# Kernel optimization log

Hardware: AMD Instinct MI355X
Metric: run time of the kernel (lower is better)

## Reference

```python
import jax, jax.numpy as jnp
import numpy as np

HIDDEN = 2048
NUM_HEADS = 8
NUM_KV_HEADS = 2
HEAD_DIM = 256
ROPE_BASE = 1e6
EPS = 1e-6
B, S = 2, 2048


def rms_norm(x, w, eps=EPS):
    # normalize over last dim (head_dim), per-head
    var = jnp.mean(jnp.square(x), axis=-1, keepdims=True)
    return x * jax.lax.rsqrt(var + eps) * w


def rope(x, positions, base=ROPE_BASE):
    # neox-style rotate-half RoPE over full head_dim. x: [B,S,H,D], positions: [B,S]
    d = x.shape[-1]
    inv_freq = 1.0 / (base ** (jnp.arange(0, d, 2, dtype=jnp.float32) / d))
    freqs = positions.astype(jnp.float32)[..., None] * inv_freq  # [B,S,D/2]
    cos = jnp.cos(freqs)[:, :, None, :]
    sin = jnp.sin(freqs)[:, :, None, :]
    x1, x2 = x[..., : d // 2], x[..., d // 2 :]
    return jnp.concatenate([x1 * cos - x2 * sin, x2 * cos + x1 * sin], axis=-1)


def setup_inputs() -> dict:
    key = jax.random.key(0)
    k1, k2, k3 = jax.random.split(key, 3)
    hidden_states = jax.random.normal(k1, (B, S, HIDDEN), dtype=jnp.float32)
    positions = jnp.broadcast_to(jnp.arange(S, dtype=jnp.int32), (B, S))
    qkv_out = (NUM_HEADS + 2 * NUM_KV_HEADS) * HEAD_DIM
    w_qkv = jax.random.normal(k2, (HIDDEN, qkv_out), dtype=jnp.float32) * (HIDDEN ** -0.5)
    w_o = jax.random.normal(k3, (NUM_HEADS * HEAD_DIM, HIDDEN), dtype=jnp.float32) * ((NUM_HEADS * HEAD_DIM) ** -0.5)
    q_norm_w = jnp.ones((HEAD_DIM,), dtype=jnp.float32)
    k_norm_w = jnp.ones((HEAD_DIM,), dtype=jnp.float32)
    return {"hidden_states": hidden_states, "positions": positions, "w_qkv": w_qkv,
            "w_o": w_o, "q_norm_w": q_norm_w, "k_norm_w": k_norm_w}


def reference(hidden_states, positions, w_qkv, w_o, q_norm_w, k_norm_w):
    b, s, _ = hidden_states.shape
    q_size = NUM_HEADS * HEAD_DIM
    kv_size = NUM_KV_HEADS * HEAD_DIM
    qkv = hidden_states @ w_qkv  # [B,S,q+2kv]
    q, k, v = jnp.split(qkv, [q_size, q_size + kv_size], axis=-1)
    q = q.reshape(b, s, NUM_HEADS, HEAD_DIM)
    k = k.reshape(b, s, NUM_KV_HEADS, HEAD_DIM)
    v = v.reshape(b, s, NUM_KV_HEADS, HEAD_DIM)
    # per-head RMSNorm; v_norm has no learned scale (weight fixed to ones)
    q = rms_norm(q, q_norm_w)
    k = rms_norm(k, k_norm_w)
    v = rms_norm(v, jnp.ones((HEAD_DIM,), dtype=v.dtype))
    # RoPE
    q = rope(q, positions)
    k = rope(k, positions)
    # GQA: repeat kv heads
    g = NUM_HEADS // NUM_KV_HEADS
    k = jnp.repeat(k, g, axis=2)
    v = jnp.repeat(v, g, axis=2)
    # causal attention with scaling = 1.0 (as in module)
    scores = jnp.einsum("bqhd,bkhd->bhqk", q, k)
    mask = jnp.tril(jnp.ones((s, s), dtype=bool))
    scores = jnp.where(mask, scores, jnp.finfo(scores.dtype).min)
    probs = jax.nn.softmax(scores, axis=-1)
    attn = jnp.einsum("bhqk,bkhd->bqhd", probs, v).reshape(b, s, NUM_HEADS * HEAD_DIM)
    return attn @ w_o
```

## Files before the change

kernel.cpp:

```cpp
#include <hip/hip_runtime.h>


#define HID  2048
#define NH   8
#define NKV  2
#define HD   256
#define SB   2048
#define BB   2
#define MTOK (BB * SB)
#define NQKV ((NH + 2 * NKV) * HD)

typedef _Float16  f16x8 __attribute__((ext_vector_type(8)));
typedef float     f32x4 __attribute__((ext_vector_type(4)));

__device__ __forceinline__ unsigned short f2h(float f) {
  _Float16 h = (_Float16)f;
  return __builtin_bit_cast(unsigned short, h);
}

__device__ __forceinline__ void async_copy16(const unsigned short* g, unsigned short* l) {
  __builtin_amdgcn_global_load_lds(
      (const __attribute__((address_space(1))) unsigned int*)g,
      (__attribute__((address_space(3))) unsigned int*)l, 16, 0, 0);
}

__device__ __forceinline__ int swz4(int r) { return (r + (r >> 2)) & 3; }

template <int OUT_MODE>
__global__ __launch_bounds__(256) void gemm_bt(const unsigned short* __restrict__ A,
                                               const unsigned short* __restrict__ Bt,
                                               void* __restrict__ Cg,
                                               int M, int N, int K) {
  __shared__ unsigned short Ash[128 * 32];
  __shared__ unsigned short Bsh[128 * 32];
  const int t = threadIdx.x;
  const int lane = t & 63, w = t >> 6;
  const int quad = lane >> 4, m15 = lane & 15;
  const int wm = w >> 1, wn = w & 1;
  const int m0 = blockIdx.y * 128, n0 = blockIdx.x * 128;

  const int rowS0 = t >> 2, rowS1 = rowS0 + 64;
  const int slot = t & 3;
  const int g0 = (slot ^ swz4(rowS0)) * 8;
  const int g1 = (slot ^ swz4(rowS1)) * 8;
  const unsigned short* Ag0 = A + (size_t)(m0 + rowS0) * K + g0;
  const unsigned short* Ag1 = A + (size_t)(m0 + rowS1) * K + g1;
  const unsigned short* Bg0 = Bt + (size_t)(n0 + rowS0) * K + g0;
  const unsigned short* Bg1 = Bt + (size_t)(n0 + rowS1) * K + g1;
  unsigned short* lA0 = &Ash[t * 8];
  unsigned short* lA1 = &Ash[(t + 256) * 8];
  unsigned short* lB0 = &Bsh[t * 8];
  unsigned short* lB1 = &Bsh[(t + 256) * 8];

  int offA[4], offB[4];
#pragma unroll
  for (int i = 0; i < 4; ++i) {
    const int ra = wm * 64 + i * 16 + m15;
    offA[i] = ra * 32 + (quad ^ swz4(ra)) * 8;
    const int rb = wn * 64 + i * 16 + m15;
    offB[i] = rb * 32 + (quad ^ swz4(rb)) * 8;
  }

  const f32x4 vz = {0.f, 0.f, 0.f, 0.f};
  f32x4 acc[4][4];
#pragma unroll
  for (int i = 0; i < 4; ++i)
#pragma unroll
    for (int j = 0; j < 4; ++j) acc[i][j] = vz;

  const int nk = K >> 5;
  for (int kt = 0; kt < nk; ++kt) {
    const int k0 = kt * 32;
    async_copy16(Ag0 + k0, lA0);
    async_copy16(Ag1 + k0, lA1);
    async_copy16(Bg0 + k0, lB0);
    async_copy16(Bg1 + k0, lB1);
    __syncthreads();
    f16x8 af[4], bfr[4];
#pragma unroll
    for (int i = 0; i < 4; ++i) af[i] = *(const f16x8*)&Ash[offA[i]];
#pragma unroll
    for (int j = 0; j < 4; ++j) bfr[j] = *(const f16x8*)&Bsh[offB[j]];
#pragma unroll
    for (int i = 0; i < 4; ++i)
#pragma unroll
      for (int j = 0; j < 4; ++j)
        acc[i][j] = __builtin_amdgcn_mfma_f32_16x16x32_f16(af[i], bfr[j], acc[i][j], 0, 0, 0);
    __syncthreads();
  }

#pragma unroll
  for (int i = 0; i < 4; ++i)
#pragma unroll
    for (int j = 0; j < 4; ++j)
#pragma unroll
      for (int r = 0; r < 4; ++r) {
        const int gm = m0 + wm * 64 + i * 16 + quad * 4 + r;
        const int gn = n0 + wn * 64 + j * 16 + m15;
        const float v = acc[i][j][r];
        if (OUT_MODE == 2) ((float*)Cg)[(size_t)gm * N + gn] = v;
        else               ((unsigned short*)Cg)[(size_t)gm * N + gn] = f2h(v);
      }
}

__global__ __launch_bounds__(256) void cvt_f32_f16(const float* __restrict__ in,
                                                   unsigned short* __restrict__ out, int n4) {
  const int i = blockIdx.x * 256 + threadIdx.x;
  if (i >= n4) return;
  const float4 v = ((const float4*)in)[i];
  ushort4 o = {f2h(v.x), f2h(v.y), f2h(v.z), f2h(v.w)};
  ((ushort4*)out)[i] = o;
}

__global__ __launch_bounds__(256) void transpose_f2h(const float* __restrict__ in,
                                                     unsigned short* __restrict__ out,
                                                     int R, int C) {
  __shared__ float tile[64 * 68];
  const int r0 = blockIdx.y * 64, c0 = blockIdx.x * 64;
  const int t = threadIdx.x;
#pragma unroll
  for (int p = 0; p < 4; ++p) {
    const int idx = t + p * 256;
    const int rr = idx >> 4, cc = (idx & 15) * 4;
    *(float4*)&tile[rr * 68 + cc] = *(const float4*)&in[(size_t)(r0 + rr) * C + c0 + cc];
  }
  __syncthreads();
#pragma unroll
  for (int p = 0; p < 2; ++p) {
    const int idx = t + p * 256;
    const int dr = idx >> 3, sc = (idx & 7) * 8;
    union { uint4 v; unsigned short s[8]; } o;
#pragma unroll
    for (int e = 0; e < 8; ++e) o.s[e] = f2h(tile[(sc + e) * 68 + dr]);
    *(uint4*)&out[(size_t)(c0 + dr) * R + r0 + sc] = o.v;
  }
}

__global__ __launch_bounds__(256) void normrope(const unsigned short* __restrict__ qkv,
                                                const int* __restrict__ pos,
                                                const float* __restrict__ qw,
                                                const float* __restrict__ kw,
                                                unsigned short* __restrict__ Qh,
                                                unsigned short* __restrict__ Kh,
                                                unsigned short* __restrict__ Vh) {
  const int tok = blockIdx.x;
  const int b = tok >> 11, s = tok & 2047;
  const int t = threadIdx.x, w = t >> 6, lane = t & 63;
  const float p = (float)pos[tok];
  const int dbase = lane * 4;
  const int s5 = s & 31;
  const int sp = (s & ~31) | (((s5 >> 2) & 3) << 3) | (((s5 >> 4) & 1) << 2) | (s5 & 3);

  for (int it = 0; it < 3; ++it) {
    const int slot = it * 4 + w;
    const unsigned short* src = qkv + (size_t)tok * NQKV + slot * 256 + dbase;
    union { uint2 u; _Float16 h[4]; } rd;
    rd.u = *(const uint2*)src;
    float y[4];
#pragma unroll
    for (int e = 0; e < 4; ++e) y[e] = (float)rd.h[e];
    float ssq = y[0] * y[0] + y[1] * y[1] + y[2] * y[2] + y[3] * y[3];
#pragma unroll
    for (int off = 1; off < 64; off <<= 1) ssq += __shfl_xor(ssq, off);
    const float rn = rsqrtf(ssq * (1.f / 256.f) + 1e-6f);

    if (slot < 8) {
#pragma unroll
      for (int e = 0; e < 4; ++e) y[e] *= rn * qw[dbase + e];
    } else if (slot < 10) {
#pragma unroll
      for (int e = 0; e < 4; ++e) y[e] *= rn * kw[dbase + e];
    } else {
#pragma unroll
      for (int e = 0; e < 4; ++e) y[e] *= rn;
    }

    unsigned short* dst;
    if (slot < 8)       dst = Qh + ((size_t)(b * NH + slot) * SB + s) * HD + dbase;
    else if (slot < 10) dst = Kh + ((size_t)(b * NKV + slot - 8) * SB + s) * HD + dbase;
    else                dst = Vh + ((size_t)(b * NKV + slot - 10) * SB + sp) * HD + dbase;

    float outv[4];
    if (slot < 10) {
      const int i0 = dbase & 127;
      const bool lo = (lane < 32);
#pragma unroll
      for (int e = 0; e < 4; ++e) {
        const float partner = __shfl_xor(y[e], 32);
        const float invf = expf(-(float)(i0 + e) * 0.10793368f);
        const float fr = p * invf;
        const float cv = cosf(fr), sv = sinf(fr);
        outv[e] = lo ? (y[e] * cv - partner * sv) : (y[e] * cv + partner * sv);
      }
    } else {
#pragma unroll
      for (int e = 0; e < 4; ++e) outv[e] = y[e];
    }
    union { uint2 u; _Float16 h[4]; } wr;
#pragma unroll
    for (int e = 0; e < 4; ++e) wr.h[e] = (_Float16)outv[e];
    *(uint2*)dst = wr.u;
  }
}

__global__ __launch_bounds__(256) void transpose_u16(const unsigned short* __restrict__ in,
                                                     unsigned short* __restrict__ out,
                                                     int R, int C, size_t ibs, size_t obs) {
  __shared__ unsigned short tile[64 * 72];
  const unsigned short* ib = in + blockIdx.z * ibs;
  unsigned short* ob = out + blockIdx.z * obs;
  const int r0 = blockIdx.y * 64, c0 = blockIdx.x * 64;
  const int t = threadIdx.x;
#pragma unroll
  for (int pck = 0; pck < 2; ++pck) {
    const int c = t + pck * 256;
    const int rr = c >> 3, cc = (c & 7) * 8;
    *(uint4*)&tile[rr * 72 + cc] = *(const uint4*)&ib[(size_t)(r0 + rr) * C + c0 + cc];
  }
  __syncthreads();
#pragma unroll
  for (int pck = 0; pck < 2; ++pck) {
    const int c = t + pck * 256;
    const int dr = c >> 3, sc = (c & 7) * 8;
    union { uint4 v; unsigned short s[8]; } o;
#pragma unroll
    for (int e = 0; e < 8; ++e) o.s[e] = tile[(sc + e) * 72 + dr];
    *(uint4*)&ob[(size_t)(c0 + dr) * R + r0 + sc] = o.v;
  }
}

__global__ __launch_bounds__(512, 2) void flash_attn(const unsigned short* __restrict__ Qh,
                                                     const unsigned short* __restrict__ Kh,
                                                     const unsigned short* __restrict__ Vt,
                                                     unsigned short* __restrict__ attn) {
  __shared__ __align__(16) unsigned char SMEM[132096];
  unsigned short* Ksh = (unsigned short*)SMEM;
  unsigned short* Vsh = (unsigned short*)(SMEM + 65536);
  float*         MLx  = (float*)(SMEM + 131072);
  float*         mergeO = (float*)SMEM;

  const int pairi = blockIdx.x;
  const int h = blockIdx.y, b = blockIdx.z;
  const int kv = h >> 2;
  const int t = threadIdx.x, w = t >> 6, lane = t & 63;
  const int wq = w & 3, team = w >> 2;
  const int quad = lane >> 4, m15 = lane & 15;

  const unsigned short* Kb = Kh + (size_t)(b * NKV + kv) * SB * HD;
  const unsigned short* Vb = Vt + (size_t)(b * NKV + kv) * HD * SB;

  const int krow = t >> 5, kchunk = t & 31;
  const int vrow = t >> 3, vchunk = t & 7;

  const f32x4 vz = {0.f, 0.f, 0.f, 0.f};

  for (int jb = 0; jb < 2; ++jb) {
    const int qt = jb ? (31 - pairi) : pairi;
    const int q0 = qt * 64, qw0 = q0 + wq * 16;
    const int qlane = qw0 + m15;

    f16x8 aq[8];
    const unsigned short* qb = Qh + ((size_t)(b * NH + h) * SB + qw0 + m15) * HD + quad * 8;
#pragma unroll
    for (int ks = 0; ks < 8; ++ks) aq[ks] = *(const f16x8*)(qb + ks * 32);

    f32x4 o[16];
#pragma unroll
    for (int i = 0; i < 16; ++i) o[i] = vz;
    float mrow = -1e30f, lrow = 0.f;

    const int nkt = (q0 + 64) >> 6;

#pragma unroll
    for (int shot = 0; shot < 4; ++shot) {
      const int r = krow + 16 * shot;
      async_copy16(Kb + (size_t)r * HD + ((kchunk ^ (r & 7)) * 8),
                   &Ksh[4096 * shot + t * 8]);
    }
#pragma unroll
    for (int shot = 0; shot < 4; ++shot) {
      const int d = vrow + 64 * shot;
      async_copy16(Vb + (size_t)d * SB + ((vchunk ^ (d & 7)) * 8),
                   &Vsh[4096 * shot + t * 8]);
    }
    __syncthreads();

    for (int kt = 0; kt < nkt; ++kt) {
      const int k0 = kt * 64;
      const int par = kt & 1;

      if (kt + 1 < nkt) {
        const int kn = k0 + 64;
        const int pn = par ^ 1;
#pragma unroll
        for (int shot = 0; shot < 4; ++shot) {
          const int r = krow + 16 * shot;
          async_copy16(Kb + (size_t)(kn + r) * HD + ((kchunk ^ (r & 7)) * 8),
                       &Ksh[pn * 16384 + 4096 * shot + t * 8]);
        }
#pragma unroll
        for (int shot = 0; shot < 4; ++shot) {
          const int d = vrow + 64 * shot;
          async_copy16(Vb + (size_t)d * SB + kn + ((vchunk ^ (d & 7)) * 8),
                       &Vsh[pn * 16384 + 4096 * shot + t * 8]);
        }
      }

      const unsigned short* KB = &Ksh[par * 16384];
      const unsigned short* VB = &Vsh[par * 16384];

      f32x4 sv[2];
      sv[0] = vz; sv[1] = vz;
#pragma unroll
      for (int g = 0; g < 2; ++g) {
        const int key = team * 32 + g * 16 + m15;
        const unsigned short* kr = &KB[key * 256];
        const int sw = (key & 7);
#pragma unroll
        for (int ks = 0; ks < 8; ++ks) {
          const f16x8 ak = *(const f16x8*)&kr[((4 * ks + quad) ^ sw) * 8];
          sv[g] = __builtin_amdgcn_mfma_f32_16x16x32_f16(ak, aq[ks], sv[g], 0, 0, 0);
        }
      }

      const bool last = (kt == nkt - 1);
      float p2[2][4];
#pragma unroll
      for (int g = 0; g < 2; ++g)
#pragma unroll
        for (int r = 0; r < 4; ++r) {
          float s = sv[g][r];
          if (last && (k0 + team * 32 + g * 16 + quad * 4 + r) > qlane) s = -3.0e38f;
          p2[g][r] = s;
        }
      float tm = fmaxf(fmaxf(fmaxf(p2[0][0], p2[0][1]), fmaxf(p2[0][2], p2[0][3])),
                       fmaxf(fmaxf(p2[1][0], p2[1][1]), fmaxf(p2[1][2], p2[1][3])));
      tm = fmaxf(tm, __shfl_xor(tm, 16));
      tm = fmaxf(tm, __shfl_xor(tm, 32));
      if (!__all(tm <= mrow)) {
        const float mnew = fmaxf(mrow, tm);
        const float alpha = __expf(mrow - mnew);
        lrow *= alpha;
#pragma unroll
        for (int dbi = 0; dbi < 16; ++dbi) o[dbi] *= alpha;
        mrow = mnew;
      }
      float rs = 0.f;
#pragma unroll
      for (int g = 0; g < 2; ++g)
#pragma unroll
        for (int r = 0; r < 4; ++r) { p2[g][r] = __expf(p2[g][r] - mrow); rs += p2[g][r]; }
      rs += __shfl_xor(rs, 16);
      rs += __shfl_xor(rs, 32);
      lrow += rs;

      f16x8 bp;
#pragma unroll
      for (int g = 0; g < 2; ++g)
#pragma unroll
        for (int r = 0; r < 4; ++r) bp[g * 4 + r] = (_Float16)p2[g][r];

#pragma unroll
      for (int dbi = 0; dbi < 16; ++dbi) {
        const int d = dbi * 16 + m15;
        const f16x8 av = *(const f16x8*)&VB[d * 64 + (((team * 4 + quad) ^ (d & 7)) * 8)];
        o[dbi] = __builtin_amdgcn_mfma_f32_16x16x32_f16(av, bp, o[dbi], 0, 0, 0);
      }

      __syncthreads();
    }

    if (quad == 0) {
      MLx[w * 32 + m15 * 2]     = mrow;
      MLx[w * 32 + m15 * 2 + 1] = lrow;
    }
    {
      float* mo = mergeO + w * 2176;
#pragma unroll
      for (int ii = 0; ii < 8; ++ii) {
        const int dbi = team ? ii : (8 + ii);
#pragma unroll
        for (int r = 0; r < 4; ++r)
          mo[(ii * 16 + quad * 4 + r) * 17 + m15] = o[dbi][r];
      }
    }
    __syncthreads();
    {
      const int pw = w ^ 4;
      const float* pmo = mergeO + pw * 2176;
      const float pm = MLx[pw * 32 + m15 * 2];
      const float pl = MLx[pw * 32 + m15 * 2 + 1];
      const float mm = fmaxf(mrow, pm);
      const float a0 = __expf(mrow - mm);
      const float a1 = __expf(pm - mm);
      const float invl = 1.0f / (a0 * lrow + a1 * pl);
      const int q = qlane;
#pragma unroll
      for (int ii = 0; ii < 8; ++ii) {
        const int dbi = team ? (8 + ii) : ii;
        union { uint2 u; _Float16 hh[4]; } st;
#pragma unroll
        for (int r = 0; r < 4; ++r) {
          const float po = pmo[(ii * 16 + quad * 4 + r) * 17 + m15];
          st.hh[r] = (_Float16)((a0 * o[dbi][r] + a1 * po) * invl);
        }
        const int dcol = team * 128 + ii * 16 + quad * 4;
        *(uint2*)&attn[(size_t)(b * SB + q) * (NH * HD) + h * HD + dcol] = st.u;
      }
    }
    __syncthreads();
  }
}

static constexpr size_t OFF_HB   = 0;
static constexpr size_t OFF_QH   = 0;
static constexpr size_t OFF_W1T  = 16777216;
static constexpr size_t OFF_KH   = 16777216;
static constexpr size_t OFF_VH   = 20971520;
static constexpr size_t OFF_VT   = 25165824;
static constexpr size_t OFF_WOT  = 29360128;
static constexpr size_t OFF_QKV  = 37748736;
static constexpr size_t OFF_ATTN = OFF_QKV;

extern "C" void kernel_launch(void* const* d_in, const int* in_sizes, int n_in,
                              void* d_out, int out_size, void* d_ws, size_t ws_size,
                              hipStream_t stream) {
  const float* hidden    = (const float*)d_in[0];
  const int*   positions = (const int*)d_in[1];
  const float* w_qkv     = (const float*)d_in[2];
  const float* w_o       = (const float*)d_in[3];
  const float* qw        = (const float*)d_in[4];
  const float* kw        = (const float*)d_in[5];
  float* out = (float*)d_out;
  char* ws = (char*)d_ws;

  unsigned short* hb    = (unsigned short*)(ws + OFF_HB);
  unsigned short* wqkvT = (unsigned short*)(ws + OFF_W1T);
  unsigned short* woT   = (unsigned short*)(ws + OFF_WOT);
  unsigned short* qkvb  = (unsigned short*)(ws + OFF_QKV);
  unsigned short* attnb = (unsigned short*)(ws + OFF_ATTN);
  unsigned short* Qhb   = (unsigned short*)(ws + OFF_QH);
  unsigned short* Khb   = (unsigned short*)(ws + OFF_KH);
  unsigned short* Vhb   = (unsigned short*)(ws + OFF_VH);
  unsigned short* Vtb   = (unsigned short*)(ws + OFF_VT);

  cvt_f32_f16<<<dim3((MTOK * HID / 4 + 255) / 256), 256, 0, stream>>>(hidden, hb, MTOK * HID / 4);
  transpose_f2h<<<dim3(NQKV / 64, HID / 64), 256, 0, stream>>>(w_qkv, wqkvT, HID, NQKV);
  transpose_f2h<<<dim3(HID / 64, HID / 64), 256, 0, stream>>>(w_o, woT, HID, HID);

  gemm_bt<0><<<dim3(NQKV / 128, MTOK / 128), 256, 0, stream>>>(hb, wqkvT, qkvb, MTOK, NQKV, HID);

  normrope<<<dim3(MTOK), 256, 0, stream>>>(qkvb, positions, qw, kw, Qhb, Khb, Vhb);

  transpose_u16<<<dim3(HD / 64, SB / 64, BB * NKV), 256, 0, stream>>>(Vhb, Vtb, SB, HD,
                                                                     (size_t)SB * HD, (size_t)SB * HD);

  flash_attn<<<dim3(16, NH, BB), 512, 0, stream>>>(Qhb, Khb, Vtb, attnb);

  gemm_bt<2><<<dim3(HID / 128, MTOK / 128), 256, 0, stream>>>(attnb, woT, out, MTOK, HID, HID);
}
```

Baseline: 343.9 us.

## Replace GEMM with 4-stage pipelined 256-row tiles and XCD-aware block remap

Replaces the single-buffered 128x128 GEMM with a 512-thread kernel using 256xBN tiles. Operand loads go straight to LDS through a 4-deep ring buffer, three stages ahead, with explicit vmcnt waits, split-phase MFMA and setprio. Blocks are remapped across 8 XCDs to improve L2 locality. The goal is to hide global load latency and raise reuse per tile. In exchange it uses more LDS and registers, and the fixed waitcnt values are fragile.

```diff
diff --git a/kernel.cpp b/kernel.cpp
--- a/kernel.cpp
+++ b/kernel.cpp
@@ -26,77 +26,146 @@
 
 __device__ __forceinline__ int swz4(int r) { return (r + (r >> 2)) & 3; }
 
-template <int OUT_MODE>
-__global__ __launch_bounds__(256) void gemm_bt(const unsigned short* __restrict__ A,
-                                               const unsigned short* __restrict__ Bt,
-                                               void* __restrict__ Cg,
-                                               int M, int N, int K) {
-  __shared__ unsigned short Ash[128 * 32];
-  __shared__ unsigned short Bsh[128 * 32];
+template <int OUT_MODE, int BN>
+__global__ __launch_bounds__(512, 2) void gemm_p2(const unsigned short* __restrict__ A,
+                                                  const unsigned short* __restrict__ Bt,
+                                                  void* __restrict__ Cg,
+                                                  int M, int N, int K) {
+  constexpr int WN  = BN / 4;
+  constexpr int NF  = BN / 64;
+  constexpr int LPTB = BN / 128;
+  __shared__ __align__(16) unsigned short Ash[4 * 256 * 32];
+  __shared__ __align__(16) unsigned short Bsh[4 * BN * 32];
+
   const int t = threadIdx.x;
   const int lane = t & 63, w = t >> 6;
   const int quad = lane >> 4, m15 = lane & 15;
-  const int wm = w >> 1, wn = w & 1;
-  const int m0 = blockIdx.y * 128, n0 = blockIdx.x * 128;
-
-  const int rowS0 = t >> 2, rowS1 = rowS0 + 64;
-  const int slot = t & 3;
-  const int g0 = (slot ^ swz4(rowS0)) * 8;
-  const int g1 = (slot ^ swz4(rowS1)) * 8;
-  const unsigned short* Ag0 = A + (size_t)(m0 + rowS0) * K + g0;
-  const unsigned short* Ag1 = A + (size_t)(m0 + rowS1) * K + g1;
-  const unsigned short* Bg0 = Bt + (size_t)(n0 + rowS0) * K + g0;
-  const unsigned short* Bg1 = Bt + (size_t)(n0 + rowS1) * K + g1;
-  unsigned short* lA0 = &Ash[t * 8];
-  unsigned short* lA1 = &Ash[(t + 256) * 8];
-  unsigned short* lB0 = &Bsh[t * 8];
-  unsigned short* lB1 = &Bsh[(t + 256) * 8];
-
-  int offA[4], offB[4];
-#pragma unroll
-  for (int i = 0; i < 4; ++i) {
-    const int ra = wm * 64 + i * 16 + m15;
-    offA[i] = ra * 32 + (quad ^ swz4(ra)) * 8;
-    const int rb = wn * 64 + i * 16 + m15;
-    offB[i] = rb * 32 + (quad ^ swz4(rb)) * 8;
+  const int wm = w >> 2, wn = w & 3;
+
+  const int nwg = gridDim.x * gridDim.y;
+  int bid = blockIdx.y * gridDim.x + blockIdx.x;
+  if ((nwg & 7) == 0) bid = (bid & 7) * (nwg >> 3) + (bid >> 3);
+  const int bx = bid % gridDim.x, by = bid / gridDim.x;
+  const int m0 = by * 256, n0 = bx * BN;
+
+  const unsigned short* aSrc[2];
+  int aDst[2];
+#pragma unroll
+  for (int j = 0; j < 2; ++j) {
+    const int c = t + j * 512;
+    const int row = c >> 2, slot = c & 3;
+    aSrc[j] = A + (size_t)(m0 + row) * K + ((slot ^ swz4(row)) * 8);
+    aDst[j] = c * 8;
+  }
+  const unsigned short* bSrc[LPTB];
+  int bDst[LPTB];
+#pragma unroll
+  for (int j = 0; j < LPTB; ++j) {
+    const int c = t + j * 512;
+    const int row = c >> 2, slot = c & 3;
+    bSrc[j] = Bt + (size_t)(n0 + row) * K + ((slot ^ swz4(row)) * 8);
+    bDst[j] = c * 8;
+  }
+
+  int offA[8], offB[NF];
+#pragma unroll
+  for (int i = 0; i < 8; ++i) {
+    const int ra = wm * 128 + i * 16 + m15;
+    offA[i] = ra * 32 + ((quad ^ swz4(ra)) * 8);
+  }
+#pragma unroll
+  for (int j = 0; j < NF; ++j) {
+    const int rb = wn * WN + j * 16 + m15;
+    offB[j] = rb * 32 + ((quad ^ swz4(rb)) * 8);
   }
 
   const f32x4 vz = {0.f, 0.f, 0.f, 0.f};
-  f32x4 acc[4][4];
-#pragma unroll
-  for (int i = 0; i < 4; ++i)
-#pragma unroll
-    for (int j = 0; j < 4; ++j) acc[i][j] = vz;
-
-  const int nk = K >> 5;
-  for (int kt = 0; kt < nk; ++kt) {
-    const int k0 = kt * 32;
-    async_copy16(Ag0 + k0, lA0);
-    async_copy16(Ag1 + k0, lA1);
-    async_copy16(Bg0 + k0, lB0);
-    async_copy16(Bg1 + k0, lB1);
-    __syncthreads();
-    f16x8 af[4], bfr[4];
-#pragma unroll
-    for (int i = 0; i < 4; ++i) af[i] = *(const f16x8*)&Ash[offA[i]];
-#pragma unroll
-    for (int j = 0; j < 4; ++j) bfr[j] = *(const f16x8*)&Bsh[offB[j]];
+  f32x4 acc[8][NF];
+#pragma unroll
+  for (int i = 0; i < 8; ++i)
+#pragma unroll
+    for (int j = 0; j < NF; ++j) acc[i][j] = vz;
+
+  const int NK = K >> 5;
+
+  for (int pt = 0; pt < 3; ++pt) {
+    const int kb = pt * 32;
+    unsigned short* ab = &Ash[pt * 8192];
+    unsigned short* bb = &Bsh[pt * (BN * 32)];
+#pragma unroll
+    for (int j = 0; j < 2; ++j) async_copy16(aSrc[j] + kb, ab + aDst[j]);
+#pragma unroll
+    for (int j = 0; j < LPTB; ++j) async_copy16(bSrc[j] + kb, bb + bDst[j]);
+  }
+  if constexpr (BN == 256) asm volatile("s_waitcnt vmcnt(8)" ::: "memory");
+  else                     asm volatile("s_waitcnt vmcnt(6)" ::: "memory");
+  __builtin_amdgcn_s_barrier();
+
+  for (int kt = 0; kt < NK; ++kt) {
+    const int buf = kt & 3;
+    const unsigned short* Ab = &Ash[buf * 8192];
+    const unsigned short* Bb = &Bsh[buf * (BN * 32)];
+    const int s3 = kt + 3;
+    const int kb3 = s3 * 32;
+    unsigned short* a3 = &Ash[(s3 & 3) * 8192];
+    unsigned short* b3 = &Bsh[(s3 & 3) * (BN * 32)];
+    const bool stage3 = (s3 < NK);
+
+    f16x8 af[4], bf[NF];
+#pragma unroll
+    for (int i = 0; i < 4; ++i) af[i] = *(const f16x8*)&Ab[offA[i]];
+#pragma unroll
+    for (int j = 0; j < NF; ++j) bf[j] = *(const f16x8*)&Bb[offB[j]];
+    if (stage3) {
+#pragma unroll
+      for (int j = 0; j < 2; ++j) async_copy16(aSrc[j] + kb3, a3 + aDst[j]);
+    }
+    __builtin_amdgcn_s_barrier();
+    asm volatile("s_waitcnt lgkmcnt(0)" ::: "memory");
+    __builtin_amdgcn_sched_barrier(0);
+    __builtin_amdgcn_s_setprio(1);
 #pragma unroll
     for (int i = 0; i < 4; ++i)
 #pragma unroll
-      for (int j = 0; j < 4; ++j)
-        acc[i][j] = __builtin_amdgcn_mfma_f32_16x16x32_f16(af[i], bfr[j], acc[i][j], 0, 0, 0);
-    __syncthreads();
-  }
-
-#pragma unroll
-  for (int i = 0; i < 4; ++i)
-#pragma unroll
-    for (int j = 0; j < 4; ++j)
+      for (int j = 0; j < NF; ++j)
+        acc[i][j] = __builtin_amdgcn_mfma_f32_16x16x32_f16(af[i], bf[j], acc[i][j], 0, 0, 0);
+    __builtin_amdgcn_s_setprio(0);
+    __builtin_amdgcn_s_barrier();
+
+    f16x8 ag[4];
+#pragma unroll
+    for (int i = 0; i < 4; ++i) ag[i] = *(const f16x8*)&Ab[offA[4 + i]];
+    if (stage3) {
+#pragma unroll
+      for (int j = 0; j < LPTB; ++j) async_copy16(bSrc[j] + kb3, b3 + bDst[j]);
+    }
+    __builtin_amdgcn_s_barrier();
+    asm volatile("s_waitcnt lgkmcnt(0)" ::: "memory");
+    __builtin_amdgcn_sched_barrier(0);
+    __builtin_amdgcn_s_setprio(1);
+#pragma unroll
+    for (int i = 0; i < 4; ++i)
+#pragma unroll
+      for (int j = 0; j < NF; ++j)
+        acc[4 + i][j] = __builtin_amdgcn_mfma_f32_16x16x32_f16(ag[i], bf[j], acc[4 + i][j], 0, 0, 0);
+    __builtin_amdgcn_s_setprio(0);
+    if (stage3) {
+      if constexpr (BN == 256) asm volatile("s_waitcnt vmcnt(8)" ::: "memory");
+      else                     asm volatile("s_waitcnt vmcnt(6)" ::: "memory");
+    } else {
+      asm volatile("s_waitcnt vmcnt(0)" ::: "memory");
+    }
+    __builtin_amdgcn_s_barrier();
+  }
+
+#pragma unroll
+  for (int i = 0; i < 8; ++i)
+#pragma unroll
+    for (int j = 0; j < NF; ++j)
 #pragma unroll
       for (int r = 0; r < 4; ++r) {
-        const int gm = m0 + wm * 64 + i * 16 + quad * 4 + r;
-        const int gn = n0 + wn * 64 + j * 16 + m15;
+        const int gm = m0 + wm * 128 + i * 16 + quad * 4 + r;
+        const int gn = n0 + wn * WN + j * 16 + m15;
         const float v = acc[i][j][r];
         if (OUT_MODE == 2) ((float*)Cg)[(size_t)gm * N + gn] = v;
         else               ((unsigned short*)Cg)[(size_t)gm * N + gn] = f2h(v);
@@ -448,7 +517,7 @@
   transpose_f2h<<<dim3(NQKV / 64, HID / 64), 256, 0, stream>>>(w_qkv, wqkvT, HID, NQKV);
   transpose_f2h<<<dim3(HID / 64, HID / 64), 256, 0, stream>>>(w_o, woT, HID, HID);
 
-  gemm_bt<0><<<dim3(NQKV / 128, MTOK / 128), 256, 0, stream>>>(hb, wqkvT, qkvb, MTOK, NQKV, HID);
+  gemm_p2<0, 256><<<dim3(NQKV / 256, MTOK / 256), 512, 0, stream>>>(hb, wqkvT, qkvb, MTOK, NQKV, HID);
 
   normrope<<<dim3(MTOK), 256, 0, stream>>>(qkvb, positions, qw, kw, Qhb, Khb, Vhb);
 
@@ -457,5 +526,5 @@
 
   flash_attn<<<dim3(16, NH, BB), 512, 0, stream>>>(Qhb, Khb, Vtb, attnb);
 
-  gemm_bt<2><<<dim3(HID / 128, MTOK / 128), 256, 0, stream>>>(attnb, woT, out, MTOK, HID, HID);
-}
+  gemm_p2<2, 128><<<dim3(HID / 128, MTOK / 256), 512, 0, stream>>>(attnb, woT, out, MTOK, HID, HID);
+}
```

New measurement: 337.7 us. No clear change (-1.8%).
